# Kernel tuning notes

Hardware: AMD Instinct MI355X
Metric: run time of the kernel (lower is better)

The kernel has to match this reference:

```python
import jax, jax.numpy as jnp
import numpy as np

B, N, D = 4, 2048, 512
H, DA, DL = 8, 64, 64  # heads, attention_dim, linear_dim
EPS = 1e-6


def _layer_norm(x, eps=EPS):
    # F.layer_norm with no affine params
    mu = jnp.mean(x, axis=-1, keepdims=True)
    var = jnp.var(x, axis=-1, keepdims=True)
    return (x - mu) * jax.lax.rsqrt(var + eps)


def setup_inputs() -> dict:
    key = jax.random.key(0)
    k1, k2, k3, k4 = jax.random.split(key, 4)
    x = jax.random.normal(k1, (B, N, D), dtype=jnp.float32)
    # causal (lower-triangular) valid-attention mask, float {0,1}, shape (B,1,N,N)
    attention_mask = jnp.broadcast_to(
        jnp.tril(jnp.ones((N, N), dtype=jnp.float32))[None, None], (B, 1, N, N)
    )
    # _uvqk: (D, 2*H*DL + 2*H*DA), init normal(0, 0.02)
    uvqk = 0.02 * jax.random.normal(k2, (D, 2 * H * DL + 2 * H * DA), dtype=jnp.float32)
    # _o: Linear(H*DL -> D), xavier uniform
    fan_in, fan_out = H * DL, D
    limit = float(np.sqrt(6.0 / (fan_in + fan_out)))
    o_weight = jax.random.uniform(k3, (fan_out, fan_in), dtype=jnp.float32, minval=-limit, maxval=limit)
    o_bias = jnp.zeros((D,), dtype=jnp.float32)
    return {"x": x, "attention_mask": attention_mask, "uvqk": uvqk,
            "o_weight": o_weight, "o_bias": o_bias}


def reference(x, attention_mask, uvqk, o_weight, o_bias):
    b, n, _ = x.shape
    normed_x = _layer_norm(x)
    mm = jax.nn.silu(normed_x @ uvqk)  # fused uvqk projection + silu
    u, v, q, k = jnp.split(mm, [H * DL, 2 * H * DL, 2 * H * DL + H * DA], axis=-1)
    qh = q.reshape(b, n, H, DA)
    kh = k.reshape(b, n, H, DA)
    vh = v.reshape(b, n, H, DL)
    # silu-activated (non-softmax) attention with mask
    qk = jnp.einsum('bnhd,bmhd->bhnm', qh, kh)
    qk = jax.nn.silu(qk) / n
    qk = qk * attention_mask  # (B,1,N,N) broadcast over heads
    attn = jnp.einsum('bhnm,bmhd->bnhd', qk, vh).reshape(b, n, H * DL)
    # gated norm + output proj + residual
    o_input = u * _layer_norm(attn)
    return o_input @ o_weight.T + o_bias + x
```

## Files before the change

kernel.cpp:

```cpp
#include <hip/hip_runtime.h>

typedef __bf16 bf16x8 __attribute__((ext_vector_type(8)));
typedef float f32x4 __attribute__((ext_vector_type(4)));
typedef float f32x16 __attribute__((ext_vector_type(16)));

__device__ __forceinline__ unsigned short f2bf(float f) {
  return __builtin_bit_cast(unsigned short, (__bf16)f);
}
__device__ __forceinline__ float bfu2f(unsigned short b) {
  unsigned int u = ((unsigned int)b) << 16;
  return __builtin_bit_cast(float, u);
}
__device__ __forceinline__ float silu_f(float x) {
  return x * __builtin_amdgcn_rcpf(1.0f + __expf(-x));
}
__device__ __forceinline__ unsigned pk2(float a, float b) {
  return (unsigned)f2bf(a) | ((unsigned)f2bf(b) << 16);
}

template<int CPR, int NI, int SWZ>
__device__ __forceinline__ void stage16(const __bf16* __restrict__ g, int ld,
                                        __bf16* lds, int wave, int lane) {
#pragma unroll
  for (int t = 0; t < NI; ++t) {
    int cb = (wave * NI + t) * 64;
    int c = cb + lane;
    int row = c / CPR;
    int colb = (c % CPR) ^ (row & SWZ);
    __builtin_amdgcn_global_load_lds(
        (const __attribute__((address_space(1))) unsigned int*)(g + row * ld + colb * 8),
        (__attribute__((address_space(3))) unsigned int*)(lds + cb * 8),
        16, 0, 0);
  }
}


__global__ void k_tr_uvqk(const float* __restrict__ uvqk, __bf16* __restrict__ uvqkT) {
  __shared__ float tile[32][33];
  int n0 = blockIdx.x * 32, k0 = blockIdx.y * 32;
  int tx = threadIdx.x, ty = threadIdx.y;
  for (int i = ty; i < 32; i += 8)
    tile[i][tx] = uvqk[(k0 + i) * 2048 + n0 + tx];
  __syncthreads();
  for (int i = ty; i < 32; i += 8)
    uvqkT[(n0 + i) * 512 + k0 + tx] = (__bf16)tile[tx][i];
}

__global__ void k_prep(const float* __restrict__ x, __bf16* __restrict__ nx,
                       const float* __restrict__ ow, __bf16* __restrict__ owb) {
  int bid = blockIdx.x, t = threadIdx.x;
  if (bid >= 8192) {
    int i = (bid - 8192) * 128 + t;
    float4 v = ((const float4*)ow)[i];
    ushort4 o4;
    o4.x = f2bf(v.x); o4.y = f2bf(v.y); o4.z = f2bf(v.z); o4.w = f2bf(v.w);
    ((ushort4*)owb)[i] = o4;
    return;
  }
  float4 v = ((const float4*)(x + (size_t)bid * 512))[t];
  float s = v.x + v.y + v.z + v.w;
  float ss = v.x * v.x + v.y * v.y + v.z * v.z + v.w * v.w;
#pragma unroll
  for (int o = 32; o > 0; o >>= 1) { s += __shfl_down(s, o); ss += __shfl_down(ss, o); }
  __shared__ float red[4];
  if ((t & 63) == 0) { red[(t >> 6) * 2] = s; red[(t >> 6) * 2 + 1] = ss; }
  __syncthreads();
  s = red[0] + red[2]; ss = red[1] + red[3];
  float mu = s * (1.0f / 512.0f);
  float var = ss * (1.0f / 512.0f) - mu * mu;
  float rs = rsqrtf(var + 1e-6f);
  ushort4 o4;
  o4.x = f2bf((v.x - mu) * rs); o4.y = f2bf((v.y - mu) * rs);
  o4.z = f2bf((v.z - mu) * rs); o4.w = f2bf((v.w - mu) * rs);
  ((ushort4*)(nx + (size_t)bid * 512))[t] = o4;
}

__global__ __launch_bounds__(256, 3) void k_proj(
    const __bf16* __restrict__ A, const __bf16* __restrict__ Bt,
    __bf16* __restrict__ u, __bf16* __restrict__ qn,
    __bf16* __restrict__ kn, __bf16* __restrict__ vt) {
  __shared__ __bf16 As[128 * 64], Bs[128 * 64];
  int tid = threadIdx.x, wave = tid >> 6, lane = tid & 63;
  int lr = lane & 15, lq = lane >> 4;
  int bn = blockIdx.x, bm = blockIdx.y;
  const __bf16* Ag = A + (size_t)bm * 128 * 512;
  const __bf16* Bg = Bt + (size_t)bn * 128 * 512;
  int wm = (wave >> 1) * 64, wn = (wave & 1) * 64;
  f32x4 acc[4][4] = {};
  for (int k0 = 0; k0 < 512; k0 += 64) {
    stage16<8, 4, 7>(Ag + k0, 512, As, wave, lane);
    stage16<8, 4, 7>(Bg + k0, 512, Bs, wave, lane);
    __syncthreads();
#pragma unroll
    for (int kk = 0; kk < 2; ++kk) {
      int b = kk * 4 + lq;
      bf16x8 a[4], bb[4];
#pragma unroll
      for (int i = 0; i < 4; ++i) {
        int row = wm + i * 16 + lr;
        a[i] = *(const bf16x8*)(As + row * 64 + ((b ^ (row & 7)) * 8));
      }
#pragma unroll
      for (int j = 0; j < 4; ++j) {
        int row = wn + j * 16 + lr;
        bb[j] = *(const bf16x8*)(Bs + row * 64 + ((b ^ (row & 7)) * 8));
      }
#pragma unroll
      for (int i = 0; i < 4; ++i)
#pragma unroll
        for (int j = 0; j < 4; ++j)
          acc[i][j] = __builtin_amdgcn_mfma_f32_16x16x32_bf16(a[i], bb[j], acc[i][j], 0, 0, 0);
    }
    __syncthreads();
  }
  int seg = bn >> 2;
  int cb = (bn & 3) * 128 + wn;
  int rb0 = bm * 128 + wm + lq * 4;
  if (seg == 1) {
#pragma unroll
    for (int i = 0; i < 4; ++i) {
      int rb = rb0 + i * 16;
      int b = rb >> 11, n = rb & 2047;
#pragma unroll
      for (int j = 0; j < 4; ++j) {
        int c = cb + j * 16 + lr;
        ushort4 w;
        w.x = f2bf(silu_f(acc[i][j][0]) * (1.0f / 2048.0f));
        w.y = f2bf(silu_f(acc[i][j][1]) * (1.0f / 2048.0f));
        w.z = f2bf(silu_f(acc[i][j][2]) * (1.0f / 2048.0f));
        w.w = f2bf(silu_f(acc[i][j][3]) * (1.0f / 2048.0f));
        *(ushort4*)(vt + ((size_t)(b * 512 + c)) * 2048 + n) = w;
      }
    }
  } else {
    __bf16* dst = (seg == 0) ? u : ((seg == 2) ? qn : kn);
#pragma unroll
    for (int i = 0; i < 4; ++i) {
      int rb = rb0 + i * 16;
#pragma unroll
      for (int j = 0; j < 4; ++j) {
        int c = cb + j * 16 + lr;
#pragma unroll
        for (int rg = 0; rg < 4; ++rg)
          dst[(size_t)(rb + rg) * 512 + c] = (__bf16)silu_f(acc[i][j][rg]);
      }
    }
  }
}

__global__ __launch_bounds__(256, 2) void k_attn(
    const __bf16* __restrict__ qn, const __bf16* __restrict__ kn,
    const __bf16* __restrict__ vt, __bf16* __restrict__ attn) {
  __shared__ __bf16 lds[36864];
  __bf16* Qs  = lds;
  __bf16* Ks0 = lds + 4096;
  __bf16* Ks1 = lds + 12288;
  __bf16* Vs0 = lds + 20480;
  __bf16* Vs1 = lds + 28672;

  int bh = blockIdx.x;
  int p = blockIdx.y;
  int half = blockIdx.z;
  int b = bh >> 3, hd = bh & 7;
  int tid = threadIdx.x, wave = tid >> 6, lane = tid & 63;
  int l31 = lane & 31, lh = lane >> 5;
  int wm = (wave >> 1) * 64, wn = (wave & 1) * 32;
  const __bf16* Kg = kn + (size_t)(b * 2048) * 512 + hd * 64;
  const __bf16* Vg = vt + (size_t)(b * 512 + hd * 64) * 2048;

  for (int ph = 0; ph < 2; ++ph) {
    int qtx = ph ? (15 - p) : p;
    int n0 = qtx * 128;
    const __bf16* Qg = qn + (size_t)(b * 2048 + n0 + half * 64) * 512 + hd * 64;
    if (ph) __syncthreads();
    stage16<8, 2, 7>(Qg, 512, Qs, wave, lane);
    stage16<8, 4, 7>(Kg, 512, Ks0, wave, lane);
    stage16<16, 4, 15>(Vg, 2048, Vs0, wave, lane);
    __syncthreads();

    bf16x8 qf[4];
#pragma unroll
    for (int ks = 0; ks < 4; ++ks) {
      int bk = (ks * 16 + lh * 8) >> 3;
      int row = wn + l31;
      qf[ks] = *(const bf16x8*)(Qs + row * 64 + ((bk ^ (row & 7)) * 8));
    }

    f32x16 po[2] = {};

    for (int mt = 0; mt <= qtx; ++mt) {
      const __bf16* Kc = (mt & 1) ? Ks1 : Ks0;
      const __bf16* Vc = (mt & 1) ? Vs1 : Vs0;
      if (mt < qtx) {
        __bf16* Kn_ = (mt & 1) ? Ks0 : Ks1;
        __bf16* Vn_ = (mt & 1) ? Vs0 : Vs1;
        stage16<8, 4, 7>(Kg + (size_t)(mt + 1) * 128 * 512, 512, Kn_, wave, lane);
        stage16<16, 4, 15>(Vg + (mt + 1) * 128, 2048, Vn_, wave, lane);
      }
      f32x16 s[2] = {};
#pragma unroll
      for (int ks = 0; ks < 4; ++ks) {
        int bk = (ks * 16 + lh * 8) >> 3;
        bf16x8 ak[2];
#pragma unroll
        for (int i = 0; i < 2; ++i) {
          int row = wm + i * 32 + l31;
          ak[i] = *(const bf16x8*)(Kc + row * 64 + ((bk ^ (row & 7)) * 8));
        }
#pragma unroll
        for (int i = 0; i < 2; ++i)
          s[i] = __builtin_amdgcn_mfma_f32_32x32x16_bf16(ak[i], qf[ks], s[i], 0, 0, 0);
      }
      bool diag = (mt == qtx);
      bool lo = (lh == 0);
      int nb = half * 64 + wn;
      bf16x8 pf[4];
#pragma unroll
      for (int i = 0; i < 2; ++i) {
        int mbase = wm + i * 32;
        bool full = diag && (mbase > nb + 31);
        unsigned pk[8];
        if (full) {
#pragma unroll
          for (int q = 0; q < 8; ++q) pk[q] = 0u;
        } else {
          bool dtile = diag && (mbase + 31 > nb);
          int mb = mbase + 4 * lh;
          int ncol = nb + l31;
          float vv[16];
#pragma unroll
          for (int r = 0; r < 16; ++r) {
            float xx = s[i][r];
            float pv = xx * __builtin_amdgcn_rcpf(1.0f + __expf(-xx));
            if (dtile) {
              int row = mb + (r & 3) + 8 * (r >> 2);
              if (row > ncol) pv = 0.0f;
            }
            vv[r] = pv;
          }
#pragma unroll
          for (int q = 0; q < 8; ++q) pk[q] = pk2(vv[2 * q], vv[2 * q + 1]);
        }
        unsigned xa = __shfl_xor(lo ? pk[2] : pk[0], 32);
        unsigned xb = __shfl_xor(lo ? pk[3] : pk[1], 32);
        unsigned xc = __shfl_xor(lo ? pk[6] : pk[4], 32);
        unsigned xd = __shfl_xor(lo ? pk[7] : pk[5], 32);
        union { bf16x8 v; unsigned u[4]; } f0, f1;
        f0.u[0] = lo ? pk[0] : xa;  f0.u[1] = lo ? pk[1] : xb;
        f0.u[2] = lo ? xa : pk[2];  f0.u[3] = lo ? xb : pk[3];
        f1.u[0] = lo ? pk[4] : xc;  f1.u[1] = lo ? pk[5] : xd;
        f1.u[2] = lo ? xc : pk[6];  f1.u[3] = lo ? xd : pk[7];
        pf[i * 2 + 0] = f0.v;
        pf[i * 2 + 1] = f1.v;
      }
#pragma unroll
      for (int t4 = 0; t4 < 4; ++t4) {
        int bk = (wm + t4 * 16 + lh * 8) >> 3;
        bf16x8 av[2];
#pragma unroll
        for (int idl = 0; idl < 2; ++idl) {
          int row = idl * 32 + l31;
          av[idl] = *(const bf16x8*)(Vc + row * 128 + ((bk ^ (row & 15)) * 8));
        }
#pragma unroll
        for (int idl = 0; idl < 2; ++idl)
          po[idl] = __builtin_amdgcn_mfma_f32_32x32x16_bf16(av[idl], pf[t4], po[idl], 0, 0, 0);
      }
      __syncthreads();
    }

    float* red = (float*)lds;
    __bf16* bo = lds + 8192;
    if (wave >= 2) {
      float* dst = red + (wave - 2) * 2048;
#pragma unroll
      for (int idl = 0; idl < 2; ++idl)
#pragma unroll
        for (int r = 0; r < 16; ++r)
          dst[(idl * 16 + r) * 64 + lane] = po[idl][r];
    }
    __syncthreads();
    if (wave < 2) {
      float* src = red + wave * 2048;
#pragma unroll
      for (int idl = 0; idl < 2; ++idl) {
#pragma unroll
        for (int r = 0; r < 16; ++r)
          po[idl][r] += src[(idl * 16 + r) * 64 + lane];
        int nrow = wn + l31;
#pragma unroll
        for (int g = 0; g < 4; ++g) {
          int dl0 = idl * 32 + g * 8 + lh * 4;
          ushort4 w;
          w.x = f2bf(po[idl][4 * g + 0]); w.y = f2bf(po[idl][4 * g + 1]);
          w.z = f2bf(po[idl][4 * g + 2]); w.w = f2bf(po[idl][4 * g + 3]);
          *(ushort4*)(bo + nrow * 72 + dl0) = w;
        }
      }
    }
    __syncthreads();
    {
      int n = tid >> 2, c0 = (tid & 3) * 16;
      __bf16* gdst = attn + (size_t)(b * 2048 + n0 + half * 64 + n) * 512 + hd * 64 + c0;
      const __bf16* lsrc = bo + n * 72 + c0;
      *(uint4*)(gdst) = *(const uint4*)(lsrc);
      *(uint4*)(gdst + 8) = *(const uint4*)(lsrc + 8);
    }
  }
}

__global__ void k_oinput(const __bf16* __restrict__ attn, const __bf16* __restrict__ u,
                         __bf16* __restrict__ oin) {
  int r = blockIdx.x, t = threadIdx.x;
  ushort4 a4 = ((const ushort4*)(attn + (size_t)r * 512))[t];
  float a0 = bfu2f(a4.x), a1 = bfu2f(a4.y), a2 = bfu2f(a4.z), a3 = bfu2f(a4.w);
  float s = a0 + a1 + a2 + a3;
  float ss = a0 * a0 + a1 * a1 + a2 * a2 + a3 * a3;
#pragma unroll
  for (int o = 32; o > 0; o >>= 1) { s += __shfl_down(s, o); ss += __shfl_down(ss, o); }
  __shared__ float red[4];
  if ((t & 63) == 0) { red[(t >> 6) * 2] = s; red[(t >> 6) * 2 + 1] = ss; }
  __syncthreads();
  s = red[0] + red[2]; ss = red[1] + red[3];
  float mu = s * (1.0f / 512.0f);
  float var = ss * (1.0f / 512.0f) - mu * mu;
  float rs = rsqrtf(var + 1e-6f);
  ushort4 u4 = ((const ushort4*)(u + (size_t)r * 512))[t];
  ushort4 o4;
  o4.x = f2bf(bfu2f(u4.x) * (a0 - mu) * rs);
  o4.y = f2bf(bfu2f(u4.y) * (a1 - mu) * rs);
  o4.z = f2bf(bfu2f(u4.z) * (a2 - mu) * rs);
  o4.w = f2bf(bfu2f(u4.w) * (a3 - mu) * rs);
  ((ushort4*)(oin + (size_t)r * 512))[t] = o4;
}

__global__ __launch_bounds__(256, 3) void k_out(
    const __bf16* __restrict__ A, const __bf16* __restrict__ Bt,
    const float* __restrict__ bias, const float* __restrict__ x,
    float* __restrict__ out) {
  __shared__ __bf16 As[128 * 64], Bs[128 * 64];
  int tid = threadIdx.x, wave = tid >> 6, lane = tid & 63;
  int lr = lane & 15, lq = lane >> 4;
  int bn = blockIdx.x, bm = blockIdx.y;
  const __bf16* Ag = A + (size_t)bm * 128 * 512;
  const __bf16* Bg = Bt + (size_t)bn * 128 * 512;
  int wm = (wave >> 1) * 64, wn = (wave & 1) * 64;
  f32x4 acc[4][4] = {};
  for (int k0 = 0; k0 < 512; k0 += 64) {
    stage16<8, 4, 7>(Ag + k0, 512, As, wave, lane);
    stage16<8, 4, 7>(Bg + k0, 512, Bs, wave, lane);
    __syncthreads();
#pragma unroll
    for (int kk = 0; kk < 2; ++kk) {
      int b = kk * 4 + lq;
      bf16x8 a[4], bb[4];
#pragma unroll
      for (int i = 0; i < 4; ++i) {
        int row = wm + i * 16 + lr;
        a[i] = *(const bf16x8*)(As + row * 64 + ((b ^ (row & 7)) * 8));
      }
#pragma unroll
      for (int j = 0; j < 4; ++j) {
        int row = wn + j * 16 + lr;
        bb[j] = *(const bf16x8*)(Bs + row * 64 + ((b ^ (row & 7)) * 8));
      }
#pragma unroll
      for (int i = 0; i < 4; ++i)
#pragma unroll
        for (int j = 0; j < 4; ++j)
          acc[i][j] = __builtin_amdgcn_mfma_f32_16x16x32_bf16(a[i], bb[j], acc[i][j], 0, 0, 0);
    }
    __syncthreads();
  }
  int cb = bn * 128 + wn;
  int rb0 = bm * 128 + wm + lq * 4;
#pragma unroll
  for (int j = 0; j < 4; ++j) {
    int c = cb + j * 16 + lr;
    float bv = bias[c];
#pragma unroll
    for (int i = 0; i < 4; ++i) {
      int rb = rb0 + i * 16;
#pragma unroll
      for (int rg = 0; rg < 4; ++rg) {
        size_t idx = (size_t)(rb + rg) * 512 + c;
        out[idx] = acc[i][j][rg] + bv + x[idx];
      }
    }
  }
}

extern "C" void kernel_launch(void* const* d_in, const int* in_sizes, int n_in,
                              void* d_out, int out_size, void* d_ws, size_t ws_size,
                              hipStream_t stream) {
  const float* x = (const float*)d_in[0];
  const float* uvqk = (const float*)d_in[2];
  const float* ow = (const float*)d_in[3];
  const float* ob = (const float*)d_in[4];
  float* out = (float*)d_out;

  char* w = (char*)d_ws;
  const size_t MB8 = 8u * 1024 * 1024;
  __bf16* nx    = (__bf16*)(w);
  __bf16* u     = (__bf16*)(w + MB8);
  __bf16* qn    = (__bf16*)(w + 2 * MB8);
  __bf16* kn    = (__bf16*)(w + 3 * MB8);
  __bf16* vt    = (__bf16*)(w + 4 * MB8);
  __bf16* uvqkT = (__bf16*)(w + 5 * MB8);
  __bf16* owb   = (__bf16*)(w + 5 * MB8 + 2097152);
  __bf16* attn  = nx;
  __bf16* o_in  = qn;

  k_tr_uvqk<<<dim3(64, 16), dim3(32, 8), 0, stream>>>(uvqk, uvqkT);
  k_prep<<<8704, 128, 0, stream>>>(x, nx, ow, owb);
  k_proj<<<dim3(16, 64), 256, 0, stream>>>(nx, uvqkT, u, qn, kn, vt);
  k_attn<<<dim3(32, 8, 2), 256, 0, stream>>>(qn, kn, vt, attn);
  k_oinput<<<8192, 128, 0, stream>>>(attn, u, o_in);
  k_out<<<dim3(4, 64), 256, 0, stream>>>(o_in, owb, ob, x, out);
}
```

Measured before the change: 202.9 us.

## Split attention KV range across two blocks with 64-row tiles and smaller LDS

The attention kernel now uses 64x64 query/key tiles instead of 128-key tiles. The causal key range of each query tile is split in two halves handled by separate blocks (z), each writing a partial result to its own buffer, with the output buffer reused as scratch for the second half. The gated-norm kernel sums both partials before normalizing. LDS drops so four blocks fit per CU and the grid doubles, improving load balance and occupancy. In exchange it adds an extra bf16 partial write/read and rounds the partials to bf16 before they are summed.

```diff
diff --git a/kernel.cpp b/kernel.cpp
--- a/kernel.cpp
+++ b/kernel.cpp
@@ -148,129 +148,115 @@
   }
 }
 
-__global__ __launch_bounds__(256, 2) void k_attn(
+__global__ __launch_bounds__(256, 4) void k_attn(
     const __bf16* __restrict__ qn, const __bf16* __restrict__ kn,
-    const __bf16* __restrict__ vt, __bf16* __restrict__ attn) {
-  __shared__ __bf16 lds[36864];
-  __bf16* Qs  = lds;
-  __bf16* Ks0 = lds + 4096;
-  __bf16* Ks1 = lds + 12288;
-  __bf16* Vs0 = lds + 20480;
-  __bf16* Vs1 = lds + 28672;
-
-  int bh = blockIdx.x;
-  int p = blockIdx.y;
-  int half = blockIdx.z;
+    const __bf16* __restrict__ vt, __bf16* __restrict__ oa,
+    __bf16* __restrict__ ob) {
+  __shared__ __bf16 lds[20480];
+  __bf16* Qs = lds;
+  __bf16* Kb0 = lds + 4096;
+  __bf16* Kb1 = lds + 8192;
+  __bf16* Vb0 = lds + 12288;
+  __bf16* Vb1 = lds + 16384;
+
+  int bh = blockIdx.x, p = blockIdx.y, z = blockIdx.z;
   int b = bh >> 3, hd = bh & 7;
   int tid = threadIdx.x, wave = tid >> 6, lane = tid & 63;
   int l31 = lane & 31, lh = lane >> 5;
-  int wm = (wave >> 1) * 64, wn = (wave & 1) * 32;
+  int wm = (wave >> 1) * 32, wn = (wave & 1) * 32;
   const __bf16* Kg = kn + (size_t)(b * 2048) * 512 + hd * 64;
   const __bf16* Vg = vt + (size_t)(b * 512 + hd * 64) * 2048;
+  __bf16* Oz = z ? ob : oa;
 
   for (int ph = 0; ph < 2; ++ph) {
-    int qtx = ph ? (15 - p) : p;
-    int n0 = qtx * 128;
-    const __bf16* Qg = qn + (size_t)(b * 2048 + n0 + half * 64) * 512 + hd * 64;
+    int t = ph ? (31 - p) : p;
+    int c0 = (t + 2) >> 1;
+    int mlo = z ? c0 : 0;
+    int cnt = (z ? (t + 1) : c0) - mlo;
+    const __bf16* Qg = qn + (size_t)(b * 2048 + t * 64) * 512 + hd * 64;
     if (ph) __syncthreads();
     stage16<8, 2, 7>(Qg, 512, Qs, wave, lane);
-    stage16<8, 4, 7>(Kg, 512, Ks0, wave, lane);
-    stage16<16, 4, 15>(Vg, 2048, Vs0, wave, lane);
+    if (cnt > 0) {
+      stage16<8, 2, 7>(Kg + (size_t)mlo * 64 * 512, 512, Kb0, wave, lane);
+      stage16<8, 2, 7>(Vg + mlo * 64, 2048, Vb0, wave, lane);
+    }
     __syncthreads();
 
     bf16x8 qf[4];
 #pragma unroll
     for (int ks = 0; ks < 4; ++ks) {
-      int bk = (ks * 16 + lh * 8) >> 3;
       int row = wn + l31;
-      qf[ks] = *(const bf16x8*)(Qs + row * 64 + ((bk ^ (row & 7)) * 8));
+      qf[ks] = *(const bf16x8*)(Qs + row * 64 + (((ks * 2 + lh) ^ (row & 7)) * 8));
     }
 
     f32x16 po[2] = {};
 
-    for (int mt = 0; mt <= qtx; ++mt) {
-      const __bf16* Kc = (mt & 1) ? Ks1 : Ks0;
-      const __bf16* Vc = (mt & 1) ? Vs1 : Vs0;
-      if (mt < qtx) {
-        __bf16* Kn_ = (mt & 1) ? Ks0 : Ks1;
-        __bf16* Vn_ = (mt & 1) ? Vs0 : Vs1;
-        stage16<8, 4, 7>(Kg + (size_t)(mt + 1) * 128 * 512, 512, Kn_, wave, lane);
-        stage16<16, 4, 15>(Vg + (mt + 1) * 128, 2048, Vn_, wave, lane);
-      }
-      f32x16 s[2] = {};
+    for (int i = 0; i < cnt; ++i) {
+      int mt = mlo + i;
+      const __bf16* Kc = (i & 1) ? Kb1 : Kb0;
+      const __bf16* Vc = (i & 1) ? Vb1 : Vb0;
+      if (i + 1 < cnt) {
+        __bf16* Kn_ = (i & 1) ? Kb0 : Kb1;
+        __bf16* Vn_ = (i & 1) ? Vb0 : Vb1;
+        stage16<8, 2, 7>(Kg + (size_t)(mt + 1) * 64 * 512, 512, Kn_, wave, lane);
+        stage16<8, 2, 7>(Vg + (mt + 1) * 64, 2048, Vn_, wave, lane);
+      }
+      f32x16 s = {};
 #pragma unroll
       for (int ks = 0; ks < 4; ++ks) {
-        int bk = (ks * 16 + lh * 8) >> 3;
-        bf16x8 ak[2];
-#pragma unroll
-        for (int i = 0; i < 2; ++i) {
-          int row = wm + i * 32 + l31;
-          ak[i] = *(const bf16x8*)(Kc + row * 64 + ((bk ^ (row & 7)) * 8));
+        int row = wm + l31;
+        bf16x8 ak = *(const bf16x8*)(Kc + row * 64 + (((ks * 2 + lh) ^ (row & 7)) * 8));
+        s = __builtin_amdgcn_mfma_f32_32x32x16_bf16(ak, qf[ks], s, 0, 0, 0);
+      }
+      bool diag = (mt == t);
+      bool full = diag && (wm > wn + 31);
+      bool dtile = diag && !full && (wm + 31 > wn);
+      unsigned pk[8];
+      if (full) {
+#pragma unroll
+        for (int q = 0; q < 8; ++q) pk[q] = 0u;
+      } else {
+        float vv[16];
+#pragma unroll
+        for (int r = 0; r < 16; ++r) {
+          float xx = s[r];
+          float pv = xx * __builtin_amdgcn_rcpf(1.0f + __expf(-xx));
+          if (dtile) {
+            int mrow = wm + 4 * lh + (r & 3) + 8 * (r >> 2);
+            int ncol = wn + l31;
+            if (mrow > ncol) pv = 0.0f;
+          }
+          vv[r] = pv;
         }
 #pragma unroll
-        for (int i = 0; i < 2; ++i)
-          s[i] = __builtin_amdgcn_mfma_f32_32x32x16_bf16(ak[i], qf[ks], s[i], 0, 0, 0);
-      }
-      bool diag = (mt == qtx);
+        for (int q = 0; q < 8; ++q) pk[q] = pk2(vv[2 * q], vv[2 * q + 1]);
+      }
       bool lo = (lh == 0);
-      int nb = half * 64 + wn;
-      bf16x8 pf[4];
-#pragma unroll
-      for (int i = 0; i < 2; ++i) {
-        int mbase = wm + i * 32;
-        bool full = diag && (mbase > nb + 31);
-        unsigned pk[8];
-        if (full) {
-#pragma unroll
-          for (int q = 0; q < 8; ++q) pk[q] = 0u;
-        } else {
-          bool dtile = diag && (mbase + 31 > nb);
-          int mb = mbase + 4 * lh;
-          int ncol = nb + l31;
-          float vv[16];
-#pragma unroll
-          for (int r = 0; r < 16; ++r) {
-            float xx = s[i][r];
-            float pv = xx * __builtin_amdgcn_rcpf(1.0f + __expf(-xx));
-            if (dtile) {
-              int row = mb + (r & 3) + 8 * (r >> 2);
-              if (row > ncol) pv = 0.0f;
-            }
-            vv[r] = pv;
-          }
-#pragma unroll
-          for (int q = 0; q < 8; ++q) pk[q] = pk2(vv[2 * q], vv[2 * q + 1]);
-        }
-        unsigned xa = __shfl_xor(lo ? pk[2] : pk[0], 32);
-        unsigned xb = __shfl_xor(lo ? pk[3] : pk[1], 32);
-        unsigned xc = __shfl_xor(lo ? pk[6] : pk[4], 32);
-        unsigned xd = __shfl_xor(lo ? pk[7] : pk[5], 32);
-        union { bf16x8 v; unsigned u[4]; } f0, f1;
-        f0.u[0] = lo ? pk[0] : xa;  f0.u[1] = lo ? pk[1] : xb;
-        f0.u[2] = lo ? xa : pk[2];  f0.u[3] = lo ? xb : pk[3];
-        f1.u[0] = lo ? pk[4] : xc;  f1.u[1] = lo ? pk[5] : xd;
-        f1.u[2] = lo ? xc : pk[6];  f1.u[3] = lo ? xd : pk[7];
-        pf[i * 2 + 0] = f0.v;
-        pf[i * 2 + 1] = f1.v;
-      }
-#pragma unroll
-      for (int t4 = 0; t4 < 4; ++t4) {
-        int bk = (wm + t4 * 16 + lh * 8) >> 3;
-        bf16x8 av[2];
+      unsigned xa = __shfl_xor(lo ? pk[2] : pk[0], 32);
+      unsigned xb = __shfl_xor(lo ? pk[3] : pk[1], 32);
+      unsigned xc = __shfl_xor(lo ? pk[6] : pk[4], 32);
+      unsigned xd = __shfl_xor(lo ? pk[7] : pk[5], 32);
+      union { bf16x8 v; unsigned u[4]; } f0, f1;
+      f0.u[0] = lo ? pk[0] : xa;  f0.u[1] = lo ? pk[1] : xb;
+      f0.u[2] = lo ? xa : pk[2];  f0.u[3] = lo ? xb : pk[3];
+      f1.u[0] = lo ? pk[4] : xc;  f1.u[1] = lo ? pk[5] : xd;
+      f1.u[2] = lo ? xc : pk[6];  f1.u[3] = lo ? xd : pk[7];
+      bf16x8 pf[2] = { f0.v, f1.v };
+#pragma unroll
+      for (int t2 = 0; t2 < 2; ++t2) {
 #pragma unroll
         for (int idl = 0; idl < 2; ++idl) {
           int row = idl * 32 + l31;
-          av[idl] = *(const bf16x8*)(Vc + row * 128 + ((bk ^ (row & 15)) * 8));
+          bf16x8 av = *(const bf16x8*)(Vc + row * 64 +
+              ((((wm >> 3) + t2 * 2 + lh) ^ (row & 7)) * 8));
+          po[idl] = __builtin_amdgcn_mfma_f32_32x32x16_bf16(av, pf[t2], po[idl], 0, 0, 0);
         }
-#pragma unroll
-        for (int idl = 0; idl < 2; ++idl)
-          po[idl] = __builtin_amdgcn_mfma_f32_32x32x16_bf16(av[idl], pf[t4], po[idl], 0, 0, 0);
       }
       __syncthreads();
     }
 
-    float* red = (float*)lds;
-    __bf16* bo = lds + 8192;
+    float* red = (float*)(Kb0);
+    __bf16* bo = Vb1;
     if (wave >= 2) {
       float* dst = red + (wave - 2) * 2048;
 #pragma unroll
@@ -282,38 +268,42 @@
     __syncthreads();
     if (wave < 2) {
       float* src = red + wave * 2048;
+      int nrow = wn + l31;
 #pragma unroll
       for (int idl = 0; idl < 2; ++idl) {
 #pragma unroll
         for (int r = 0; r < 16; ++r)
           po[idl][r] += src[(idl * 16 + r) * 64 + lane];
-        int nrow = wn + l31;
 #pragma unroll
         for (int g = 0; g < 4; ++g) {
           int dl0 = idl * 32 + g * 8 + lh * 4;
+          int addr = nrow * 64 + ((((dl0 >> 3) ^ (nrow & 7)) << 3) | (dl0 & 7));
           ushort4 w;
           w.x = f2bf(po[idl][4 * g + 0]); w.y = f2bf(po[idl][4 * g + 1]);
           w.z = f2bf(po[idl][4 * g + 2]); w.w = f2bf(po[idl][4 * g + 3]);
-          *(ushort4*)(bo + nrow * 72 + dl0) = w;
+          *(ushort4*)(bo + addr) = w;
         }
       }
     }
     __syncthreads();
     {
-      int n = tid >> 2, c0 = (tid & 3) * 16;
-      __bf16* gdst = attn + (size_t)(b * 2048 + n0 + half * 64 + n) * 512 + hd * 64 + c0;
-      const __bf16* lsrc = bo + n * 72 + c0;
-      *(uint4*)(gdst) = *(const uint4*)(lsrc);
-      *(uint4*)(gdst + 8) = *(const uint4*)(lsrc + 8);
-    }
-  }
-}
-
-__global__ void k_oinput(const __bf16* __restrict__ attn, const __bf16* __restrict__ u,
-                         __bf16* __restrict__ oin) {
+      int n = tid >> 2, cc = (tid & 3) * 16;
+      __bf16* gdst = Oz + (size_t)(b * 2048 + t * 64 + n) * 512 + hd * 64 + cc;
+      int a0 = n * 64 + (((cc >> 3) ^ (n & 7)) << 3);
+      int a1 = n * 64 + ((((cc >> 3) + 1) ^ (n & 7)) << 3);
+      *(uint4*)(gdst) = *(const uint4*)(bo + a0);
+      *(uint4*)(gdst + 8) = *(const uint4*)(bo + a1);
+    }
+  }
+}
+
+__global__ void k_oinput(const __bf16* __restrict__ oa, const __bf16* __restrict__ ob,
+                         const __bf16* __restrict__ u, __bf16* __restrict__ oin) {
   int r = blockIdx.x, t = threadIdx.x;
-  ushort4 a4 = ((const ushort4*)(attn + (size_t)r * 512))[t];
-  float a0 = bfu2f(a4.x), a1 = bfu2f(a4.y), a2 = bfu2f(a4.z), a3 = bfu2f(a4.w);
+  ushort4 a4 = ((const ushort4*)(oa + (size_t)r * 512))[t];
+  ushort4 b4 = ((const ushort4*)(ob + (size_t)r * 512))[t];
+  float a0 = bfu2f(a4.x) + bfu2f(b4.x), a1 = bfu2f(a4.y) + bfu2f(b4.y);
+  float a2 = bfu2f(a4.z) + bfu2f(b4.z), a3 = bfu2f(a4.w) + bfu2f(b4.w);
   float s = a0 + a1 + a2 + a3;
   float ss = a0 * a0 + a1 * a1 + a2 * a2 + a3 * a3;
 #pragma unroll
@@ -396,7 +386,7 @@
   const float* x = (const float*)d_in[0];
   const float* uvqk = (const float*)d_in[2];
   const float* ow = (const float*)d_in[3];
-  const float* ob = (const float*)d_in[4];
+  const float* obias = (const float*)d_in[4];
   float* out = (float*)d_out;
 
   char* w = (char*)d_ws;
@@ -408,13 +398,14 @@
   __bf16* vt    = (__bf16*)(w + 4 * MB8);
   __bf16* uvqkT = (__bf16*)(w + 5 * MB8);
   __bf16* owb   = (__bf16*)(w + 5 * MB8 + 2097152);
-  __bf16* attn  = nx;
+  __bf16* Oa    = nx;
+  __bf16* Ob    = (__bf16*)d_out;
   __bf16* o_in  = qn;
 
   k_tr_uvqk<<<dim3(64, 16), dim3(32, 8), 0, stream>>>(uvqk, uvqkT);
   k_prep<<<8704, 128, 0, stream>>>(x, nx, ow, owb);
   k_proj<<<dim3(16, 64), 256, 0, stream>>>(nx, uvqkT, u, qn, kn, vt);
-  k_attn<<<dim3(32, 8, 2), 256, 0, stream>>>(qn, kn, vt, attn);
-  k_oinput<<<8192, 128, 0, stream>>>(attn, u, o_in);
-  k_out<<<dim3(4, 64), 256, 0, stream>>>(o_in, owb, ob, x, out);
-}
+  k_attn<<<dim3(32, 16, 2), 256, 0, stream>>>(qn, kn, vt, Oa, Ob);
+  k_oinput<<<8192, 128, 0, stream>>>(Oa, Ob, u, o_in);
+  k_out<<<dim3(4, 64), 256, 0, stream>>>(o_in, owb, obias, x, out);
+}
```

New measurement: 210.3 us. +3.6%, slower.
